# Kernel optimization log

Measured on AMD Instinct MI355X. Metric: run time of the kernel, lower is better.

Reference implementation:

```python
import jax, jax.numpy as jnp
import numpy as np

B, F0, D = 2048, 40, 32
LAYER0, LAYER1 = 128, 128  # layer_size=(128,128), split_half=True -> field_nums=[40,64]


def setup_inputs() -> dict:
    key = jax.random.key(0)
    k1, k2, k3 = jax.random.split(key, 3)
    x = jax.random.normal(k1, (B, F0, D), dtype=jnp.float32)
    # TF conv1d filters: [1, F_prev*F0, size]; we store them reshaped [F0, F_prev_fields, size]
    # Layer 0: F_prev = F0 = 40 -> W0 flattened index m = i*F0 + j, i over x0 fields, j over hidden fields
    W0 = jax.random.normal(k2, (F0, F0, LAYER0), dtype=jnp.float32) * 0.05
    b0 = jnp.zeros((LAYER0,), dtype=jnp.float32)
    # Layer 1: F_prev = LAYER0 // 2 = 64 (split_half)
    W1 = jax.random.normal(k3, (F0, LAYER0 // 2, LAYER1), dtype=jnp.float32) * 0.05
    b1 = jnp.zeros((LAYER1,), dtype=jnp.float32)
    return {"x": x, "W0": W0, "b0": b0, "W1": W1, "b1": b1}


def reference(x, W0, b0, W1, b1):
    # CIN layer 0: outer product x0 (x) x0 over fields per embedding dim, then 1x1 conv + bias + relu
    # TF flattens dot_result as index i*F_prev + j, matching W0[i, j, s].
    h0 = jax.nn.relu(jnp.einsum('bid,bjd,ijs->bsd', x, x, W0) + b0[None, :, None])  # (B, 128, D)
    half = LAYER0 // 2
    next_hidden, direct0 = h0[:, :half, :], h0[:, half:, :]  # split_half
    # CIN layer 1 (last layer): all feature maps go to direct connect
    direct1 = jax.nn.relu(
        jnp.einsum('bid,bjd,ijs->bsd', x, next_hidden, W1) + b1[None, :, None]
    )  # (B, 128, D)
    result = jnp.concatenate([direct0, direct1], axis=1)  # (B, 192, D)
    return jnp.sum(result, axis=-1)  # (B, 192)
```

## Files before the change

### kernel.cpp

```cpp
#include <hip/hip_runtime.h>
#include <stdint.h>


typedef __attribute__((ext_vector_type(8))) _Float16 half8;
typedef __attribute__((ext_vector_type(2))) _Float16 half2v;
typedef __attribute__((ext_vector_type(4))) float f32x4;

__device__ __forceinline__ unsigned short f2h(float f) {
    return __builtin_bit_cast(unsigned short, (_Float16)f);
}
__device__ __forceinline__ float qsum(float v) {
    v += __shfl_xor(v, 16, 64);
    v += __shfl_xor(v, 32, 64);
    return v;
}

__global__ void permute_w_both(const float* __restrict__ W0, const float* __restrict__ W1,
                               unsigned short* __restrict__ Wp0, unsigned short* __restrict__ Wp1)
{
    int t = blockIdx.x;
    int s = threadIdx.x >> 1, h = threadIdx.x & 1;
    const float* W; unsigned short* Wp; int JW, tt;
    if (t < 50) { W = W0; Wp = Wp0; JW = 40; tt = t; }
    else        { W = W1; Wp = Wp1; JW = 64; tt = t - 50; }
    int jc = tt / 10, ic = tt - jc * 10;
    unsigned short outv[16];
    #pragma unroll
    for (int q = 0; q < 16; ++q) {
        int kl = h * 16 + q;
        int i = ic * 4 + (kl >> 3), j = jc * 8 + (kl & 7);
        outv[q] = f2h(W[((size_t)(i * JW + j)) * 128 + s]);
    }
    unsigned short* dst = Wp + (size_t)tt * 4096 + s * 32 + h * 16;
    *(uint4*)dst       = *(const uint4*)outv;
    *(uint4*)(dst + 8) = *(const uint4*)(outv + 8);
}

template<int NJC>
__device__ __forceinline__ void gemm_phase(
    const unsigned short* __restrict__ Wp,
    const unsigned short* __restrict__ Jl,
    int jstride,
    const unsigned int xi2[4][10],
    unsigned short* Wb,
    f32x4 acc[4][4], int tid)
{
    constexpr int T = NJC * 10;
    const int lane = tid & 63;
    const int rt = (tid >> 6) & 3;
    const int sh = tid >> 8;
    const int ml = lane & 15;
    const int kc = lane >> 4;

    const unsigned short* jrow[4];
    #pragma unroll
    for (int mt = 0; mt < 4; ++mt)
        jrow[mt] = Jl + (rt * 64 + mt * 16 + ml) * jstride;

    const unsigned short* brd = Wb + (sh * 64 + ml) * 32 + kc * 8;
    unsigned short* bwr = Wb + tid * 8;

    uint4 wrn;
    {
        uint4 w0 = *(const uint4*)(Wp + tid * 8);
        *(uint4*)bwr = w0;
        wrn = *(const uint4*)(Wp + 4096 + tid * 8);
    }
    uint4 jv[4], jvn[4];
    #pragma unroll
    for (int mt = 0; mt < 4; ++mt) jv[mt] = *(const uint4*)(jrow[mt]);
    __syncthreads();

    for (int jc = 0; jc < NJC; ++jc) {
        if (jc + 1 < NJC) {
            #pragma unroll
            for (int mt = 0; mt < 4; ++mt) jvn[mt] = *(const uint4*)(jrow[mt] + (jc + 1) * 8);
        } else {
            #pragma unroll
            for (int mt = 0; mt < 4; ++mt) jvn[mt] = jv[mt];
        }
        #pragma unroll
        for (int ic = 0; ic < 10; ++ic) {
            const int tt = jc * 10 + ic;
            const int cb = ic & 1;
            const int nb = cb ^ 1;
            if (tt + 1 < T) *(uint4*)(bwr + nb * 4096) = wrn;
            {
                const unsigned short* wg =
                    Wp + (size_t)((tt + 2 < T) ? (tt + 2) : tt) * 4096 + tid * 8;
                wrn = *(const uint4*)wg;
            }
            uint4 bv[4];
            #pragma unroll
            for (int nt = 0; nt < 4; ++nt)
                bv[nt] = *(const uint4*)(brd + cb * 4096 + nt * 512);
            uint4 av[4];
            #pragma unroll
            for (int mt = 0; mt < 4; ++mt) {
                half2v x2 = __builtin_bit_cast(half2v, xi2[mt][ic]);
                av[mt].x = __builtin_bit_cast(unsigned int,
                    (half2v)(x2 * __builtin_bit_cast(half2v, jv[mt].x)));
                av[mt].y = __builtin_bit_cast(unsigned int,
                    (half2v)(x2 * __builtin_bit_cast(half2v, jv[mt].y)));
                av[mt].z = __builtin_bit_cast(unsigned int,
                    (half2v)(x2 * __builtin_bit_cast(half2v, jv[mt].z)));
                av[mt].w = __builtin_bit_cast(unsigned int,
                    (half2v)(x2 * __builtin_bit_cast(half2v, jv[mt].w)));
            }
            #pragma unroll
            for (int mt = 0; mt < 4; ++mt)
                #pragma unroll
                for (int nt = 0; nt < 4; ++nt)
                    acc[mt][nt] = __builtin_amdgcn_mfma_f32_16x16x32_f16(
                        __builtin_bit_cast(half8, av[mt]),
                        __builtin_bit_cast(half8, bv[nt]),
                        acc[mt][nt], 0, 0, 0);
            __syncthreads();
        }
        #pragma unroll
        for (int mt = 0; mt < 4; ++mt) jv[mt] = jvn[mt];
    }
}

__global__ __launch_bounds__(512, 2)
void fused_two_layer(const float* __restrict__ x,
                     const unsigned short* __restrict__ W0p,
                     const float* __restrict__ b0,
                     const unsigned short* __restrict__ W1p,
                     const float* __restrict__ b1,
                     float* __restrict__ out)
{
    __shared__ __align__(16) unsigned short Xl[256 * 40];
    __shared__ __align__(16) unsigned short NH[256 * 72];
    __shared__ __align__(16) unsigned short Wb[2 * 4096];

    const int tid  = threadIdx.x;
    const int lane = tid & 63;
    const int rt   = (tid >> 6) & 3;
    const int sh   = tid >> 8;
    const int ml   = lane & 15;
    const int kc   = lane >> 4;

    const float* xblk = x + (size_t)blockIdx.x * (8 * 40 * 32);
    #pragma unroll
    for (int bl = 0; bl < 8; ++bl) {
        #pragma unroll
        for (int k = 0; k < 3; ++k) {
            int f = 512 * k + tid;
            if (f < 1280) {
                int i = f >> 5, d = f & 31;
                Xl[(bl * 32 + d) * 40 + i] = f2h(xblk[bl * 1280 + f]);
            }
        }
    }
    __syncthreads();

    unsigned int xi2[4][10];
    #pragma unroll
    for (int mt = 0; mt < 4; ++mt) {
        const unsigned short* xr = Xl + (rt * 64 + mt * 16 + ml) * 40;
        #pragma unroll
        for (int ic = 0; ic < 10; ++ic) {
            unsigned int u = xr[ic * 4 + kc];
            xi2[mt][ic] = u | (u << 16);
        }
    }

    f32x4 acc[4][4];
    const f32x4 zero4 = {0.f, 0.f, 0.f, 0.f};
    #pragma unroll
    for (int mt = 0; mt < 4; ++mt)
        #pragma unroll
        for (int nt = 0; nt < 4; ++nt) acc[mt][nt] = zero4;

    gemm_phase<5>(W0p, Xl, 40, xi2, Wb, acc, tid);

    {
        float bias[4];
        #pragma unroll
        for (int nt = 0; nt < 4; ++nt) bias[nt] = b0[sh * 64 + nt * 16 + ml];
        if (sh == 0) {
            #pragma unroll
            for (int mt = 0; mt < 4; ++mt) {
                int r = rt * 64 + mt * 16 + (kc << 2);
                #pragma unroll
                for (int nt = 0; nt < 4; ++nt) {
                    int s = nt * 16 + ml;
                    #pragma unroll
                    for (int rg = 0; rg < 4; ++rg) {
                        float v = fmaxf(acc[mt][nt][rg] + bias[nt], 0.0f);
                        NH[(r + rg) * 72 + s] = f2h(v);
                    }
                }
            }
        } else {
            int bb = blockIdx.x * 8 + rt * 2;
            #pragma unroll
            for (int nt = 0; nt < 4; ++nt) {
                float sA = 0.f, sB = 0.f;
                #pragma unroll
                for (int rg = 0; rg < 4; ++rg) {
                    sA += fmaxf(acc[0][nt][rg] + bias[nt], 0.f) + fmaxf(acc[1][nt][rg] + bias[nt], 0.f);
                    sB += fmaxf(acc[2][nt][rg] + bias[nt], 0.f) + fmaxf(acc[3][nt][rg] + bias[nt], 0.f);
                }
                sA = qsum(sA); sB = qsum(sB);
                if (lane < 16) {
                    int col = nt * 16 + lane;
                    out[(size_t)bb * 192 + col]       = sA;
                    out[(size_t)(bb + 1) * 192 + col] = sB;
                }
            }
        }
    }
    __syncthreads();

    #pragma unroll
    for (int mt = 0; mt < 4; ++mt)
        #pragma unroll
        for (int nt = 0; nt < 4; ++nt) acc[mt][nt] = zero4;

    gemm_phase<8>(W1p, NH, 72, xi2, Wb, acc, tid);

    {
        float bias[4];
        #pragma unroll
        for (int nt = 0; nt < 4; ++nt) bias[nt] = b1[sh * 64 + nt * 16 + ml];
        int bb = blockIdx.x * 8 + rt * 2;
        #pragma unroll
        for (int nt = 0; nt < 4; ++nt) {
            float sA = 0.f, sB = 0.f;
            #pragma unroll
            for (int rg = 0; rg < 4; ++rg) {
                sA += fmaxf(acc[0][nt][rg] + bias[nt], 0.f) + fmaxf(acc[1][nt][rg] + bias[nt], 0.f);
                sB += fmaxf(acc[2][nt][rg] + bias[nt], 0.f) + fmaxf(acc[3][nt][rg] + bias[nt], 0.f);
            }
            sA = qsum(sA); sB = qsum(sB);
            if (lane < 16) {
                int col = 64 + sh * 64 + nt * 16 + lane;
                out[(size_t)bb * 192 + col]       = sA;
                out[(size_t)(bb + 1) * 192 + col] = sB;
            }
        }
    }
}

extern "C" void kernel_launch(void* const* d_in, const int* in_sizes, int n_in,
                              void* d_out, int out_size, void* d_ws, size_t ws_size,
                              hipStream_t stream) {
    const float* x  = (const float*)d_in[0];
    const float* W0 = (const float*)d_in[1];
    const float* b0 = (const float*)d_in[2];
    const float* W1 = (const float*)d_in[3];
    const float* b1 = (const float*)d_in[4];
    float* out = (float*)d_out;

    unsigned short* W0p = (unsigned short*)d_ws;
    unsigned short* W1p = (unsigned short*)((char*)d_ws + 50 * 4096 * 2);

    permute_w_both<<<130, 256, 0, stream>>>(W0, W1, W0p, W1p);
    fused_two_layer<<<256, 512, 0, stream>>>(x, W0p, b0, W1p, b1, out);
}
```

Baseline: 131.3 us.

## Stage five weight tiles per LDS buffer to cut barriers in CIN GEMM

The weight staging in the fused CIN GEMM moves from one 4096-element tile per double-buffer slot to five tiles per slot. This allows one __syncthreads per five MFMA tiles instead of one per tile, and prefetches five tiles of global weights into registers at a time. The cost is a much larger LDS footprint (about 80KB of weight buffers) and more live registers. Both could reduce occupancy below the two blocks per CU requested by the launch bounds. The per-chunk prefetch of the j-row vectors is also removed, so they are now loaded directly each chunk.

```diff
diff --git a/kernel.cpp b/kernel.cpp
--- a/kernel.cpp
+++ b/kernel.cpp
@@ -35,6 +35,8 @@
     *(uint4*)dst       = *(const uint4*)outv;
     *(uint4*)(dst + 8) = *(const uint4*)(outv + 8);
 }
+
+#define WBUF 20480
 
 template<int NJC>
 __device__ __forceinline__ void gemm_phase(
@@ -60,65 +62,71 @@
     const unsigned short* brd = Wb + (sh * 64 + ml) * 32 + kc * 8;
     unsigned short* bwr = Wb + tid * 8;
 
-    uint4 wrn;
+    uint4 wr[5];
     {
-        uint4 w0 = *(const uint4*)(Wp + tid * 8);
-        *(uint4*)bwr = w0;
-        wrn = *(const uint4*)(Wp + 4096 + tid * 8);
-    }
-    uint4 jv[4], jvn[4];
-    #pragma unroll
-    for (int mt = 0; mt < 4; ++mt) jv[mt] = *(const uint4*)(jrow[mt]);
+        uint4 w0[5];
+        #pragma unroll
+        for (int u = 0; u < 5; ++u)
+            w0[u] = *(const uint4*)(Wp + (size_t)u * 4096 + tid * 8);
+        #pragma unroll
+        for (int u = 0; u < 5; ++u)
+            *(uint4*)(bwr + u * 4096) = w0[u];
+        #pragma unroll
+        for (int u = 0; u < 5; ++u)
+            wr[u] = *(const uint4*)(Wp + (size_t)(5 + u) * 4096 + tid * 8);
+    }
     __syncthreads();
 
-    for (int jc = 0; jc < NJC; ++jc) {
-        if (jc + 1 < NJC) {
-            #pragma unroll
-            for (int mt = 0; mt < 4; ++mt) jvn[mt] = *(const uint4*)(jrow[mt] + (jc + 1) * 8);
-        } else {
-            #pragma unroll
-            for (int mt = 0; mt < 4; ++mt) jvn[mt] = jv[mt];
-        }
-        #pragma unroll
-        for (int ic = 0; ic < 10; ++ic) {
-            const int tt = jc * 10 + ic;
-            const int cb = ic & 1;
-            const int nb = cb ^ 1;
-            if (tt + 1 < T) *(uint4*)(bwr + nb * 4096) = wrn;
-            {
-                const unsigned short* wg =
-                    Wp + (size_t)((tt + 2 < T) ? (tt + 2) : tt) * 4096 + tid * 8;
-                wrn = *(const uint4*)wg;
-            }
-            uint4 bv[4];
-            #pragma unroll
-            for (int nt = 0; nt < 4; ++nt)
-                bv[nt] = *(const uint4*)(brd + cb * 4096 + nt * 512);
-            uint4 av[4];
-            #pragma unroll
-            for (int mt = 0; mt < 4; ++mt) {
-                half2v x2 = __builtin_bit_cast(half2v, xi2[mt][ic]);
-                av[mt].x = __builtin_bit_cast(unsigned int,
-                    (half2v)(x2 * __builtin_bit_cast(half2v, jv[mt].x)));
-                av[mt].y = __builtin_bit_cast(unsigned int,
-                    (half2v)(x2 * __builtin_bit_cast(half2v, jv[mt].y)));
-                av[mt].z = __builtin_bit_cast(unsigned int,
-                    (half2v)(x2 * __builtin_bit_cast(half2v, jv[mt].z)));
-                av[mt].w = __builtin_bit_cast(unsigned int,
-                    (half2v)(x2 * __builtin_bit_cast(half2v, jv[mt].w)));
-            }
-            #pragma unroll
-            for (int mt = 0; mt < 4; ++mt)
+    for (int jc2 = 0; jc2 < NJC; ++jc2) {
+        uint4 jv[4];
+        #pragma unroll
+        for (int mt = 0; mt < 4; ++mt) jv[mt] = *(const uint4*)(jrow[mt] + jc2 * 8);
+
+        #pragma unroll
+        for (int half = 0; half < 2; ++half) {
+            const int cb = half;
+            const int nb = half ^ 1;
+            const int t0 = jc2 * 10 + half * 5;
+            #pragma unroll
+            for (int u = 0; u < 5; ++u)
+                *(uint4*)(bwr + nb * WBUF + u * 4096) = wr[u];
+            #pragma unroll
+            for (int u = 0; u < 5; ++u) {
+                int tl = t0 + 10 + u;
+                if (tl >= T) tl = t0 + u;
+                wr[u] = *(const uint4*)(Wp + (size_t)tl * 4096 + tid * 8);
+            }
+            #pragma unroll
+            for (int u = 0; u < 5; ++u) {
+                const int ic = half * 5 + u;
+                uint4 bv[4];
                 #pragma unroll
                 for (int nt = 0; nt < 4; ++nt)
-                    acc[mt][nt] = __builtin_amdgcn_mfma_f32_16x16x32_f16(
-                        __builtin_bit_cast(half8, av[mt]),
-                        __builtin_bit_cast(half8, bv[nt]),
-                        acc[mt][nt], 0, 0, 0);
+                    bv[nt] = *(const uint4*)(brd + cb * WBUF + u * 4096 + nt * 512);
+                uint4 av[4];
+                #pragma unroll
+                for (int mt = 0; mt < 4; ++mt) {
+                    half2v x2 = __builtin_bit_cast(half2v, xi2[mt][ic]);
+                    av[mt].x = __builtin_bit_cast(unsigned int,
+                        (half2v)(x2 * __builtin_bit_cast(half2v, jv[mt].x)));
+                    av[mt].y = __builtin_bit_cast(unsigned int,
+                        (half2v)(x2 * __builtin_bit_cast(half2v, jv[mt].y)));
+                    av[mt].z = __builtin_bit_cast(unsigned int,
+                        (half2v)(x2 * __builtin_bit_cast(half2v, jv[mt].z)));
+                    av[mt].w = __builtin_bit_cast(unsigned int,
+                        (half2v)(x2 * __builtin_bit_cast(half2v, jv[mt].w)));
+                }
+                #pragma unroll
+                for (int mt = 0; mt < 4; ++mt)
+                    #pragma unroll
+                    for (int nt = 0; nt < 4; ++nt)
+                        acc[mt][nt] = __builtin_amdgcn_mfma_f32_16x16x32_f16(
+                            __builtin_bit_cast(half8, av[mt]),
+                            __builtin_bit_cast(half8, bv[nt]),
+                            acc[mt][nt], 0, 0, 0);
+            }
             __syncthreads();
         }
-        #pragma unroll
-        for (int mt = 0; mt < 4; ++mt) jv[mt] = jvn[mt];
     }
 }
 
@@ -132,7 +140,7 @@
 {
     __shared__ __align__(16) unsigned short Xl[256 * 40];
     __shared__ __align__(16) unsigned short NH[256 * 72];
-    __shared__ __align__(16) unsigned short Wb[2 * 4096];
+    __shared__ __align__(16) unsigned short Wb[2 * WBUF];
 
     const int tid  = threadIdx.x;
     const int lane = tid & 63;
```

Measured after the change: 160.4 us. +22.1%, slower.
